# Performance work log

Measured on AMD Instinct MI355X. Metric: run time of the kernel, lower is better.

## Reference

```python
import jax, jax.numpy as jnp
import numpy as np

WEIGHTS = (0.5, 1.0, 2.0)   # per-channel weights (init kwarg)
INVERTED = True             # init kwarg


def setup_inputs() -> dict:
    key = jax.random.key(0)
    B, C, H, W = 16, 3, 256, 256
    # binary flood mask: nonzero = foreground (scipy EDT measures distance to nearest zero)
    flood = jax.random.randint(key, (B, C, H, W), 0, 2).astype(jnp.float32)
    return {"flood_batch": flood}


def _edt_squared(mask):
    """Exact squared Euclidean distance transform per [H,W] slice.

    mask: bool [B,C,H,W], True = foreground (nonzero). Returns float32 [B,C,H,W]
    squared distance from each True pixel to the nearest False pixel (0 at False).
    Uses the exact separable decomposition:
      D2[r,w] = min_{r'} ( g[r',w]^2 + (r-r')^2 ),  g = 1D horizontal distance to zero.
    """
    B, C, H, W = mask.shape
    BIG = jnp.float32(H + W)  # exceeds any achievable 1D distance

    # --- pass 1: 1D distance to nearest zero along W (forward + backward scans) ---
    m = jnp.moveaxis(mask, -1, 0)  # [W,B,C,H]

    def step(carry, mm):
        d = jnp.where(mm, jnp.minimum(carry + 1.0, BIG), 0.0)
        return d, d

    init = jnp.full((B, C, H), BIG, jnp.float32)
    _, fwd = jax.lax.scan(step, init, m)
    _, bwd = jax.lax.scan(step, init, m[::-1])
    g = jnp.minimum(fwd, bwd[::-1])          # [W,B,C,H]
    g2 = jnp.moveaxis(g, 0, -1) ** 2          # [B,C,H,W]

    # --- pass 2: exact min-plus over rows (vectorized over B,C,W; scan over output row) ---
    rows = jnp.arange(H, dtype=jnp.float32)

    def row_step(_, r):
        cand = g2 + ((r - rows) ** 2)[None, None, :, None]  # [B,C,H,W]
        return None, cand.min(axis=2)                        # [B,C,W]

    _, d2 = jax.lax.scan(row_step, None, rows)  # [H,B,C,W]
    return jnp.moveaxis(d2, 0, 2)               # [B,C,H,W]


def reference(flood_batch):
    w = jnp.asarray(WEIGHTS, jnp.float32)
    dt = jnp.sqrt(_edt_squared(flood_batch != 0))            # [B,C,H,W]
    dt = dt * w[None, :, None, None]                         # per-channel weight
    mx = dt.max(axis=(2, 3), keepdims=True)                  # per-slice max
    safe = jnp.where(mx > 0, mx, 1.0)
    scaled = (mx - dt) / safe if INVERTED else dt / safe
    return jnp.where(mx > 0, scaled, dt)
```

## Files before the change

kernel.cpp:

```cpp
#include <hip/hip_runtime.h>


#define BIGD 512.0f
#define PADV 1e30f

__global__ __launch_bounds__(256) void k1_bitmask(const float* __restrict__ in,
                                                  unsigned long long* __restrict__ bits) {
    int row = blockIdx.x * 4 + (threadIdx.x >> 6);
    int lane = threadIdx.x & 63;
    const float4 m = ((const float4*)in)[(long)row * 64 + lane];

    unsigned long long b0 = __ballot(m.x == 0.f);
    unsigned long long b1 = __ballot(m.y == 0.f);
    unsigned long long b2 = __ballot(m.z == 0.f);
    unsigned long long b3 = __ballot(m.w == 0.f);
    if (lane == 0) {
        ulonglong4* dst = (ulonglong4*)(bits + (long)row * 4);
        ulonglong4 v; v.x = b0; v.y = b1; v.z = b2; v.w = b3;
        *dst = v;
    }
}

__global__ __launch_bounds__(256) void k2_colpass(const unsigned long long* __restrict__ bits,
                                                  float* __restrict__ d2out,
                                                  float* __restrict__ stripmax) {
    __shared__ unsigned long long bm[1024];
    __shared__ float tile[16 * 289];
    __shared__ float wm[4];
    int bx = blockIdx.x;
    int slice = bx >> 4;
    int w0 = (bx & 15) * 16;
    int tid = threadIdx.x;

    {
        const unsigned long long* src = bits + (long)slice * 1024;
        #pragma unroll
        for (int i = 0; i < 4; ++i) bm[i * 256 + tid] = src[i * 256 + tid];
    }
    {
        int c = tid >> 4, i = tid & 15;
        tile[c * 289 + i] = PADV;
        tile[c * 289 + 272 + i] = PADV;
    }
    __syncthreads();

    int c = tid & 15;
    int p = w0 + c;
    int rg = tid >> 4;

    auto nz2 = [&](int row) -> float {
        int dist = 512;
        #pragma unroll
        for (int cc = 0; cc < 4; ++cc) {
            unsigned long long M = bm[row * 4 + cc];
            int q = p - cc;
            int qa = (q < 0) ? 0 : q;
            int tp = qa >> 2;
            unsigned long long Ml = (q >= 0) ? (M & (~0ull >> (63 - tp))) : 0ull;
            int tn = (q < 0) ? 0 : ((q + 3) >> 2);
            unsigned long long Mh = (tn < 64) ? (M & (~0ull << tn)) : 0ull;
            if (Ml) dist = min(dist, q - 4 * (63 - __builtin_clzll(Ml)));
            if (Mh) dist = min(dist, 4 * __builtin_ctzll(Mh) - q);
        }
        float fd = (float)dist;
        return fd * fd;
    };

    #pragma unroll
    for (int k = 0; k < 16; ++k) {
        int r = rg + 16 * k;
        tile[c * 289 + 16 + r] = nz2(r);
    }
    __syncthreads();

    int r0 = rg * 16;
    float s[48];
    #pragma unroll
    for (int i = 0; i < 48; ++i) s[i] = tile[c * 289 + r0 + i];

    float dmin[16];
    #pragma unroll
    for (int k = 0; k < 16; ++k) dmin[k] = s[k + 16];
    #pragma unroll
    for (int o = -16; o <= 16; ++o) {
        if (o == 0) continue;
        float oo = (float)(o * o);
        #pragma unroll
        for (int k = 0; k < 16; ++k)
            dmin[k] = fminf(dmin[k], s[k + 16 + o] + oo);
    }

    #pragma unroll
    for (int k = 0; k < 16; ++k) {
        if (dmin[k] > 288.0f) {
            float best = dmin[k];
            int r = r0 + k;
            for (int rp = 0; rp < 256; ++rp) {
                float dr = (float)(r - rp);
                best = fminf(best, fmaf(dr, dr, tile[c * 289 + 16 + rp]));
            }
            dmin[k] = best;
        }
    }

    float* dst = d2out + (long)slice * 65536 + w0 + c;
    float m = 0.f;
    #pragma unroll
    for (int k = 0; k < 16; ++k) {
        dst[(long)(r0 + k) * 256] = dmin[k];
        m = fmaxf(m, dmin[k]);
    }
    #pragma unroll
    for (int off = 32; off >= 1; off >>= 1)
        m = fmaxf(m, __shfl_down(m, off, 64));
    if ((tid & 63) == 0) wm[tid >> 6] = m;
    __syncthreads();
    if (tid == 0)
        stripmax[bx] = fmaxf(fmaxf(wm[0], wm[1]), fmaxf(wm[2], wm[3]));
}

__global__ __launch_bounds__(256) void k3_final(float* __restrict__ out,
                                                const float* __restrict__ stripmax) {
    __shared__ float sMx;
    int tid = threadIdx.x;
    int idx4 = blockIdx.x * 256 + tid;
    int slice = blockIdx.x >> 6;
    if (tid < 16) {
        float v = stripmax[slice * 16 + tid];
        #pragma unroll
        for (int off = 8; off >= 1; off >>= 1) v = fmaxf(v, __shfl_down(v, off, 64));
        if (tid == 0) sMx = v;
    }
    __syncthreads();

    int c = slice % 3;
    float wgt = (c == 0) ? 0.5f : ((c == 1) ? 1.0f : 2.0f);
    float mx = wgt * __builtin_sqrtf(sMx);

    float4 d2 = ((float4*)out)[idx4];
    float4 r;
    if (mx > 0.f) {
        float inv = 1.0f / mx;
        r.x = (mx - wgt * __builtin_sqrtf(d2.x)) * inv;
        r.y = (mx - wgt * __builtin_sqrtf(d2.y)) * inv;
        r.z = (mx - wgt * __builtin_sqrtf(d2.z)) * inv;
        r.w = (mx - wgt * __builtin_sqrtf(d2.w)) * inv;
    } else {
        r.x = wgt * __builtin_sqrtf(d2.x);
        r.y = wgt * __builtin_sqrtf(d2.y);
        r.z = wgt * __builtin_sqrtf(d2.z);
        r.w = wgt * __builtin_sqrtf(d2.w);
    }
    ((float4*)out)[idx4] = r;
}

extern "C" void kernel_launch(void* const* d_in, const int* in_sizes, int n_in,
                              void* d_out, int out_size, void* d_ws, size_t ws_size,
                              hipStream_t stream) {
    const float* in = (const float*)d_in[0];
    float* out = (float*)d_out;
    float* stripmax = (float*)d_ws;
    unsigned long long* bits = (unsigned long long*)((char*)d_ws + 4096);

    k1_bitmask<<<3072, 256, 0, stream>>>(in, bits);
    k2_colpass<<<768, 256, 0, stream>>>(bits, out, stripmax);
    k3_final<<<3072, 256, 0, stream>>>(out, stripmax);
}
```

Measured before the change: 83.49 us.

## Fuse normalization into column pass using per-slice atomic max and spin barrier

Merges the final normalization kernel into the column-pass kernel. Each block publishes its strip maximum through an atomicMax on a per-slice counter, then spins until all 16 blocks of its slice have arrived before normalizing and writing the output directly from registers. This removes one kernel launch and the write and re-read of the intermediate squared-distance buffer. In exchange it relies on all 16 blocks of a slice being co-resident, which risks deadlock if they are not scheduled together, and it adds spin-wait latency.

```diff
diff --git a/kernel.cpp b/kernel.cpp
--- a/kernel.cpp
+++ b/kernel.cpp
@@ -1,11 +1,13 @@
 #include <hip/hip_runtime.h>
 
 
-#define BIGD 512.0f
 #define PADV 1e30f
 
 __global__ __launch_bounds__(256) void k1_bitmask(const float* __restrict__ in,
-                                                  unsigned long long* __restrict__ bits) {
+                                                  unsigned long long* __restrict__ bits,
+                                                  unsigned* __restrict__ ctrl) {
+    if (blockIdx.x == 0 && threadIdx.x < 128) ctrl[threadIdx.x] = 0u;
+
     int row = blockIdx.x * 4 + (threadIdx.x >> 6);
     int lane = threadIdx.x & 63;
     const float4 m = ((const float4*)in)[(long)row * 64 + lane];
@@ -21,12 +23,13 @@
     }
 }
 
-__global__ __launch_bounds__(256) void k2_colpass(const unsigned long long* __restrict__ bits,
-                                                  float* __restrict__ d2out,
-                                                  float* __restrict__ stripmax) {
+__global__ __launch_bounds__(256, 3) void k2_fused(const unsigned long long* __restrict__ bits,
+                                                   float* __restrict__ out,
+                                                   unsigned* __restrict__ ctrl) {
     __shared__ unsigned long long bm[1024];
     __shared__ float tile[16 * 289];
     __shared__ float wm[4];
+    __shared__ float sMx;
     int bx = blockIdx.x;
     int slice = bx >> 4;
     int w0 = (bx & 15) * 16;
@@ -38,9 +41,9 @@
         for (int i = 0; i < 4; ++i) bm[i * 256 + tid] = src[i * 256 + tid];
     }
     {
-        int c = tid >> 4, i = tid & 15;
-        tile[c * 289 + i] = PADV;
-        tile[c * 289 + 272 + i] = PADV;
+        int cc = tid >> 4, i = tid & 15;
+        tile[cc * 289 + i] = PADV;
+        tile[cc * 289 + 272 + i] = PADV;
     }
     __syncthreads();
 
@@ -103,55 +106,43 @@
         }
     }
 
-    float* dst = d2out + (long)slice * 65536 + w0 + c;
     float m = 0.f;
     #pragma unroll
-    for (int k = 0; k < 16; ++k) {
-        dst[(long)(r0 + k) * 256] = dmin[k];
-        m = fmaxf(m, dmin[k]);
-    }
+    for (int k = 0; k < 16; ++k) m = fmaxf(m, dmin[k]);
     #pragma unroll
     for (int off = 32; off >= 1; off >>= 1)
         m = fmaxf(m, __shfl_down(m, off, 64));
     if ((tid & 63) == 0) wm[tid >> 6] = m;
     __syncthreads();
-    if (tid == 0)
-        stripmax[bx] = fmaxf(fmaxf(wm[0], wm[1]), fmaxf(wm[2], wm[3]));
-}
 
-__global__ __launch_bounds__(256) void k3_final(float* __restrict__ out,
-                                                const float* __restrict__ stripmax) {
-    __shared__ float sMx;
-    int tid = threadIdx.x;
-    int idx4 = blockIdx.x * 256 + tid;
-    int slice = blockIdx.x >> 6;
-    if (tid < 16) {
-        float v = stripmax[slice * 16 + tid];
-        #pragma unroll
-        for (int off = 8; off >= 1; off >>= 1) v = fmaxf(v, __shfl_down(v, off, 64));
-        if (tid == 0) sMx = v;
+    if (tid == 0) {
+        float bmax = fmaxf(fmaxf(wm[0], wm[1]), fmaxf(wm[2], wm[3]));
+        atomicMax(ctrl + slice, __float_as_uint(bmax));
+        __threadfence();
+        atomicAdd(ctrl + 64 + slice, 1u);
+        while (__hip_atomic_load(ctrl + 64 + slice, __ATOMIC_ACQUIRE,
+                                 __HIP_MEMORY_SCOPE_AGENT) < 16u) {
+            __builtin_amdgcn_s_sleep(1);
+        }
+        sMx = __uint_as_float(__hip_atomic_load(ctrl + slice, __ATOMIC_RELAXED,
+                                                __HIP_MEMORY_SCOPE_AGENT));
     }
     __syncthreads();
 
-    int c = slice % 3;
-    float wgt = (c == 0) ? 0.5f : ((c == 1) ? 1.0f : 2.0f);
+    int ch = slice % 3;
+    float wgt = (ch == 0) ? 0.5f : ((ch == 1) ? 1.0f : 2.0f);
     float mx = wgt * __builtin_sqrtf(sMx);
-
-    float4 d2 = ((float4*)out)[idx4];
-    float4 r;
+    float* dst = out + (long)slice * 65536 + w0 + c;
     if (mx > 0.f) {
         float inv = 1.0f / mx;
-        r.x = (mx - wgt * __builtin_sqrtf(d2.x)) * inv;
-        r.y = (mx - wgt * __builtin_sqrtf(d2.y)) * inv;
-        r.z = (mx - wgt * __builtin_sqrtf(d2.z)) * inv;
-        r.w = (mx - wgt * __builtin_sqrtf(d2.w)) * inv;
+        #pragma unroll
+        for (int k = 0; k < 16; ++k)
+            dst[(long)(r0 + k) * 256] = (mx - wgt * __builtin_sqrtf(dmin[k])) * inv;
     } else {
-        r.x = wgt * __builtin_sqrtf(d2.x);
-        r.y = wgt * __builtin_sqrtf(d2.y);
-        r.z = wgt * __builtin_sqrtf(d2.z);
-        r.w = wgt * __builtin_sqrtf(d2.w);
+        #pragma unroll
+        for (int k = 0; k < 16; ++k)
+            dst[(long)(r0 + k) * 256] = wgt * __builtin_sqrtf(dmin[k]);
     }
-    ((float4*)out)[idx4] = r;
 }
 
 extern "C" void kernel_launch(void* const* d_in, const int* in_sizes, int n_in,
@@ -159,10 +150,9 @@
                               hipStream_t stream) {
     const float* in = (const float*)d_in[0];
     float* out = (float*)d_out;
-    float* stripmax = (float*)d_ws;
+    unsigned* ctrl = (unsigned*)d_ws;
     unsigned long long* bits = (unsigned long long*)((char*)d_ws + 4096);
 
-    k1_bitmask<<<3072, 256, 0, stream>>>(in, bits);
-    k2_colpass<<<768, 256, 0, stream>>>(bits, out, stripmax);
-    k3_final<<<3072, 256, 0, stream>>>(out, stripmax);
+    k1_bitmask<<<3072, 256, 0, stream>>>(in, bits, ctrl);
+    k2_fused<<<768, 256, 0, stream>>>(bits, out, ctrl);
 }
```

Measured after the change: 102.9 us. +23.2%, slower.

## Compute own row strip in registers and alias bitmask into tile LDS

Applied to the files above, without the earlier changes.

The column-pass kernel now precomputes the per-column bit masks once, computes the horizontal distances for its own 16 contiguous rows directly into registers (rotated row order, vector LDS reads of the bitmask), and reuses them in the windowed min instead of reloading from shared memory. The bitmask buffer is aliased onto the tile buffer to cut LDS footprint, and waves_per_eu is hinted to raise occupancy. This adds an extra barrier and a different LDS access pattern, and it may raise register pressure.

```diff
diff --git a/kernel.cpp b/kernel.cpp
--- a/kernel.cpp
+++ b/kernel.cpp
@@ -1,7 +1,6 @@
 #include <hip/hip_runtime.h>
 
 
-#define BIGD 512.0f
 #define PADV 1e30f
 
 __global__ __launch_bounds__(256) void k1_bitmask(const float* __restrict__ in,
@@ -21,12 +20,14 @@
     }
 }
 
-__global__ __launch_bounds__(256) void k2_colpass(const unsigned long long* __restrict__ bits,
-                                                  float* __restrict__ d2out,
-                                                  float* __restrict__ stripmax) {
-    __shared__ unsigned long long bm[1024];
-    __shared__ float tile[16 * 289];
+__global__ __launch_bounds__(256) __attribute__((amdgpu_waves_per_eu(4)))
+void k2_colpass(const unsigned long long* __restrict__ bits,
+                float* __restrict__ d2out,
+                float* __restrict__ stripmax) {
+    __shared__ __align__(16) float tile[16 * 289];
     __shared__ float wm[4];
+    unsigned long long* bm = (unsigned long long*)tile;
+
     int bx = blockIdx.x;
     int slice = bx >> 4;
     int w0 = (bx & 15) * 16;
@@ -37,57 +38,78 @@
         #pragma unroll
         for (int i = 0; i < 4; ++i) bm[i * 256 + tid] = src[i * 256 + tid];
     }
-    {
-        int c = tid >> 4, i = tid & 15;
-        tile[c * 289 + i] = PADV;
-        tile[c * 289 + 272 + i] = PADV;
-    }
     __syncthreads();
 
     int c = tid & 15;
     int p = w0 + c;
     int rg = tid >> 4;
+    int r0 = rg * 16;
 
-    auto nz2 = [&](int row) -> float {
+    unsigned long long mLo[4], mHi[4];
+    int qv[4];
+    #pragma unroll
+    for (int cc = 0; cc < 4; ++cc) {
+        int q = p - cc;
+        int qa = (q < 0) ? 0 : q;
+        int tp = qa >> 2;
+        mLo[cc] = (q >= 0) ? (~0ull >> (63 - tp)) : 0ull;
+        int tn = (q < 0) ? 0 : ((q + 3) >> 2);
+        mHi[cc] = (tn < 64) ? (~0ull << tn) : 0ull;
+        qv[cc] = q;
+    }
+
+    const ulonglong2* bmv = (const ulonglong2*)bm;
+    float own[16];
+    #pragma unroll
+    for (int k = 0; k < 16; ++k) {
+        int kk = (k + rg) & 15;
+        int r = r0 + kk;
+        ulonglong2 wa = bmv[r * 2];
+        ulonglong2 wb = bmv[r * 2 + 1];
+        unsigned long long M[4] = { wa.x, wa.y, wb.x, wb.y };
         int dist = 512;
         #pragma unroll
         for (int cc = 0; cc < 4; ++cc) {
-            unsigned long long M = bm[row * 4 + cc];
-            int q = p - cc;
-            int qa = (q < 0) ? 0 : q;
-            int tp = qa >> 2;
-            unsigned long long Ml = (q >= 0) ? (M & (~0ull >> (63 - tp))) : 0ull;
-            int tn = (q < 0) ? 0 : ((q + 3) >> 2);
-            unsigned long long Mh = (tn < 64) ? (M & (~0ull << tn)) : 0ull;
-            if (Ml) dist = min(dist, q - 4 * (63 - __builtin_clzll(Ml)));
-            if (Mh) dist = min(dist, 4 * __builtin_ctzll(Mh) - q);
+            unsigned long long Ml = M[cc] & mLo[cc];
+            unsigned long long Mh = M[cc] & mHi[cc];
+            if (Ml) dist = min(dist, qv[cc] - 4 * (63 - __builtin_clzll(Ml)));
+            if (Mh) dist = min(dist, 4 * __builtin_ctzll(Mh) - qv[cc]);
         }
         float fd = (float)dist;
-        return fd * fd;
-    };
-
-    #pragma unroll
-    for (int k = 0; k < 16; ++k) {
-        int r = rg + 16 * k;
-        tile[c * 289 + 16 + r] = nz2(r);
+        own[kk] = fd * fd;
     }
     __syncthreads();
 
-    int r0 = rg * 16;
-    float s[48];
+    {
+        int cc = tid >> 4, i = tid & 15;
+        tile[cc * 289 + i] = PADV;
+        tile[cc * 289 + 272 + i] = PADV;
+    }
     #pragma unroll
-    for (int i = 0; i < 48; ++i) s[i] = tile[c * 289 + r0 + i];
+    for (int k = 0; k < 16; ++k)
+        tile[c * 289 + 16 + r0 + k] = own[k];
+    __syncthreads();
+
+    float lo[16], hi[16];
+    #pragma unroll
+    for (int i = 0; i < 16; ++i) {
+        lo[i] = tile[c * 289 + r0 + i];
+        hi[i] = tile[c * 289 + 32 + r0 + i];
+    }
 
     float dmin[16];
     #pragma unroll
-    for (int k = 0; k < 16; ++k) dmin[k] = s[k + 16];
+    for (int k = 0; k < 16; ++k) dmin[k] = own[k];
     #pragma unroll
-    for (int o = -16; o <= 16; ++o) {
-        if (o == 0) continue;
+    for (int o = 1; o <= 16; ++o) {
         float oo = (float)(o * o);
         #pragma unroll
-        for (int k = 0; k < 16; ++k)
-            dmin[k] = fminf(dmin[k], s[k + 16 + o] + oo);
+        for (int k = 0; k < 16; ++k) {
+            int jm = k - o, jp = k + o;
+            float a = (jm >= 0) ? own[jm] : lo[jm + 16];
+            float b = (jp < 16) ? own[jp] : hi[jp - 16];
+            dmin[k] = fminf(dmin[k], fminf(a, b) + oo);
+        }
     }
 
     #pragma unroll
```

New measurement: 86.59 us. 3.7% more time.
